# Kernel optimization log

Hardware: AMD Instinct MI355X
Metric: run time of the kernel (lower is better)

The kernel has to match this reference:

```python
import jax, jax.numpy as jnp
import numpy as np

HIDDEN = 1024
HEADS = 16
HEAD_DIM = HIDDEN // HEADS
EPS = 1e-6


def _layernorm(x, gamma, beta):
    mu = jnp.mean(x, axis=-1, keepdims=True)
    var = jnp.mean(jnp.square(x - mu), axis=-1, keepdims=True)
    return (x - mu) * jax.lax.rsqrt(var + EPS) * gamma + beta


def setup_inputs() -> dict:
    key = jax.random.key(0)
    ks = jax.random.split(key, 16)
    B, S, D = 2, 2048, HIDDEN
    s = 1.0 / np.sqrt(D)
    inp = {
        "x": jax.random.normal(ks[0], (B, S, D), dtype=jnp.float32),
        "Wq": jax.random.uniform(ks[1], (D, D), jnp.float32, -s, s),
        "bq": jnp.zeros((D,), jnp.float32),
        "Wk": jax.random.uniform(ks[2], (D, D), jnp.float32, -s, s),
        "bk": jnp.zeros((D,), jnp.float32),
        "Wv": jax.random.uniform(ks[3], (D, D), jnp.float32, -s, s),
        "bv": jnp.zeros((D,), jnp.float32),
        "Wo": jax.random.uniform(ks[4], (D, D), jnp.float32, -s, s),
        "bo": jnp.zeros((D,), jnp.float32),
        "g1": jnp.ones((D,), jnp.float32),
        "b1": jnp.zeros((D,), jnp.float32),
        "Wup": jax.random.uniform(ks[5], (D, 4 * D), jnp.float32, -s, s),
        "bup": jnp.zeros((4 * D,), jnp.float32),
        "Wdn": jax.random.uniform(ks[6], (4 * D, D), jnp.float32, -0.5 * s, 0.5 * s),
        "bdn": jnp.zeros((D,), jnp.float32),
        "g2": jnp.ones((D,), jnp.float32),
        "b2": jnp.zeros((D,), jnp.float32),
    }
    return inp


def _forward(x, Wq, bq, Wk, bk, Wv, bv, Wo, bo, g1, b1, Wup, bup, Wdn, bdn, g2, b2):
    B, S, D = x.shape
    H, Hd = HEADS, HEAD_DIM
    # projections -> (B, H, S, Hd)
    q = (x @ Wq + bq).reshape(B, S, H, Hd).transpose(0, 2, 1, 3)
    k = (x @ Wk + bk).reshape(B, S, H, Hd).transpose(0, 2, 1, 3)
    v = (x @ Wv + bv).reshape(B, S, H, Hd).transpose(0, 2, 1, 3)
    # full NxN scores (faithful to the source: explicit QK^T, mask, softmax, AV)
    scores = jnp.einsum("bhqd,bhkd->bhqk", q, k) / np.sqrt(Hd)
    causal = jnp.tril(jnp.ones((S, S), dtype=bool))  # (S, S)
    scores = jnp.where(causal, scores, jnp.float32(-1e20))
    attn = jax.nn.softmax(scores, axis=-1)
    # dropout is identity in eval mode
    mid = jnp.einsum("bhqk,bhkd->bqhd", attn, v).reshape(B, S, D)
    attn_out = mid @ Wo + bo
    x = _layernorm(x + attn_out, g1, b1)
    # FFN
    up = jax.nn.relu(x @ Wup + bup)
    down = up @ Wdn + bdn
    return _layernorm(x + down, g2, b2)


def reference(x, Wq, bq, Wk, bk, Wv, bv, Wo, bo, g1, b1, Wup, bup, Wdn, bdn, g2, b2):
    return _forward(x, Wq, bq, Wk, bk, Wv, bv, Wo, bo, g1, b1, Wup, bup, Wdn, bdn, g2, b2)
```

## Files before the change

kernel.cpp:

```cpp
#include <hip/hip_runtime.h>

#define D_MODEL 1024
#define D_FFN   4096
#define SEQ     2048
#define NROWS   4096
#define QKV_LD  3072

typedef __bf16 bf16x8 __attribute__((ext_vector_type(8)));
typedef float  floatx4 __attribute__((ext_vector_type(4)));

#define MFMA_BF16 __builtin_amdgcn_mfma_f32_16x16x32_bf16

__device__ __forceinline__ unsigned short f2bf(float f) {
  unsigned int u = __float_as_uint(f);
  u += 0x7FFFu + ((u >> 16) & 1u);
  return (unsigned short)(u >> 16);
}

template <int C>
__device__ __forceinline__ float ror16(float x) {
  return __int_as_float(
      __builtin_amdgcn_mov_dpp(__float_as_int(x), 0x120 | C, 0xf, 0xf, true));
}

__device__ __forceinline__ void async16(const unsigned short* g, unsigned short* l) {
  __builtin_amdgcn_global_load_lds(
      (const __attribute__((address_space(1))) unsigned int*)g,
      (__attribute__((address_space(3))) unsigned int*)l, 16, 0, 0);
}

__global__ __launch_bounds__(256) void k_f32_to_bf16(
    const float* __restrict__ in, unsigned short* __restrict__ outp, long n) {
  long i = ((long)blockIdx.x * 256 + threadIdx.x) * 4;
  if (i >= n) return;
  float4 v = *(const float4*)(in + i);
  ushort4 o;
  o.x = f2bf(v.x); o.y = f2bf(v.y); o.z = f2bf(v.z); o.w = f2bf(v.w);
  *(ushort4*)(outp + i) = o;
}

__global__ __launch_bounds__(256) void k_transpose_bf16(
    const float* __restrict__ W, unsigned short* __restrict__ WT, int R, int C) {
  __shared__ float tile[32][33];
  int tx = threadIdx.x & 31, ty = threadIdx.x >> 5;
  long bx = (long)blockIdx.x * 32;
  long by = (long)blockIdx.y * 32;
  #pragma unroll
  for (int j = 0; j < 4; j++)
    tile[ty + j * 8][tx] = W[(by + ty + j * 8) * C + bx + tx];
  __syncthreads();
  #pragma unroll
  for (int j = 0; j < 4; j++)
    WT[(bx + ty + j * 8) * R + by + tx] = f2bf(tile[tx][ty + j * 8]);
}

__global__ __launch_bounds__(256) void k_transpose_sq(
    const float* __restrict__ Wq, const float* __restrict__ Wk,
    const float* __restrict__ Wv, const float* __restrict__ Wo,
    unsigned short* __restrict__ WqkvT, unsigned short* __restrict__ WoT) {
  __shared__ float tile[32][33];
  int z = blockIdx.z;
  const float* W = (z == 0) ? Wq : (z == 1) ? Wk : (z == 2) ? Wv : Wo;
  unsigned short* dst = (z < 3) ? (WqkvT + (size_t)z * D_MODEL * D_MODEL) : WoT;
  int tx = threadIdx.x & 31, ty = threadIdx.x >> 5;
  long bx = (long)blockIdx.x * 32;
  long by = (long)blockIdx.y * 32;
  #pragma unroll
  for (int j = 0; j < 4; j++)
    tile[ty + j * 8][tx] = W[(by + ty + j * 8) * D_MODEL + bx + tx];
  __syncthreads();
  #pragma unroll
  for (int j = 0; j < 4; j++)
    dst[(bx + ty + j * 8) * D_MODEL + by + tx] = f2bf(tile[tx][ty + j * 8]);
}

__global__ __launch_bounds__(256) void k_pack_bias(
    const float* __restrict__ bq, const float* __restrict__ bk,
    const float* __restrict__ bv, float* __restrict__ dst) {
  int i = blockIdx.x * 256 + threadIdx.x;
  if (i >= 3072) return;
  float v = (i < 1024) ? bq[i] : (i < 2048) ? bk[i - 1024] : bv[i - 2048];
  dst[i] = v;
}

__global__ __launch_bounds__(256) void k_transpose_v(
    const unsigned short* __restrict__ QKV, unsigned short* __restrict__ Vt) {
  __shared__ unsigned short tile[64][72];
  int r0 = blockIdx.x * 64;
  int c0 = blockIdx.y * 64;
  int tx = threadIdx.x & 15, ty = threadIdx.x >> 4;
  #pragma unroll
  for (int j = 0; j < 4; j++) {
    int r = ty + j * 16;
    *(ushort4*)&tile[r][tx * 4] =
        *(const ushort4*)(QKV + (long)(r0 + r) * QKV_LD + 2048 + c0 + tx * 4);
  }
  __syncthreads();
  #pragma unroll
  for (int j = 0; j < 4; j++) {
    int d = ty + j * 16;
    ushort4 o;
    o.x = tile[tx * 4 + 0][d];
    o.y = tile[tx * 4 + 1][d];
    o.z = tile[tx * 4 + 2][d];
    o.w = tile[tx * 4 + 3][d];
    *(ushort4*)(Vt + (long)(c0 + d) * NROWS + r0 + tx * 4) = o;
  }
}

__global__ __launch_bounds__(512, 4) void k_gemm128(
    const unsigned short* __restrict__ A,
    const unsigned short* __restrict__ Bt,
    const float* __restrict__ bias,
    void* __restrict__ Cp, int M, int N, int K, int flags) {
  __shared__ unsigned short lds[2 * 16384];
  int tid = threadIdx.x, lane = tid & 63, wave = tid >> 6;
  int quad = lane >> 4, l16 = lane & 15;
  int wm = wave >> 2, wn = wave & 3;

  int gx = gridDim.x;
  int nwg = gx * gridDim.y;
  int orig = blockIdx.y * gx + blockIdx.x;
  int wg = (orig & 7) * (nwg >> 3) + (orig >> 3);
  long bm = (long)(wg % gx) * 128;
  long bn = (long)(wg / gx) * 128;

  int T = K / 64;

  const floatx4 fz = {0.f, 0.f, 0.f, 0.f};
  floatx4 acc[4][2];
  #pragma unroll
  for (int i = 0; i < 4; i++)
    #pragma unroll
    for (int j = 0; j < 2; j++) acc[i][j] = fz;

  int srow = tid >> 3;
  int sc = (tid & 7) ^ (srow & 7);
  const unsigned short* Ag = A + (bm + srow) * (long)K + sc * 8;
  const unsigned short* Bg = Bt + (bn + srow) * (long)K + sc * 8;

  auto stage = [&](int tt, int c) {
    unsigned short* An = lds + c * 16384;
    unsigned short* Bn = An + 8192;
    long ko = (long)tt * 64;
    async16(Ag + ko, An + wave * 512);
    async16(Ag + 64 * (long)K + ko, An + 4096 + wave * 512);
    async16(Bg + ko, Bn + wave * 512);
    async16(Bg + 64 * (long)K + ko, Bn + 4096 + wave * 512);
  };

  int aoff = (wm * 64 + l16) * 64;
  int boff = (wn * 32 + l16) * 64;
  int sw = l16 & 7;
  int ca0 = (quad ^ sw) * 8;
  int ca1 = ((4 + quad) ^ sw) * 8;

  stage(0, 0);
  for (int t = 0; t < T; t++) {
    int c = t & 1;
    const unsigned short* Ac = lds + c * 16384;
    const unsigned short* Bc = Ac + 8192;
    int tn = (t + 1 < T) ? t + 1 : T - 1;
    stage(tn, c ^ 1);
    __asm__ volatile("s_waitcnt vmcnt(4)" ::: "memory");
    __builtin_amdgcn_s_barrier();

    bf16x8 af[4][2], bfr[2][2];
    #pragma unroll
    for (int m = 0; m < 4; m++) {
      af[m][0] = *(const bf16x8*)(Ac + aoff + m * 1024 + ca0);
      af[m][1] = *(const bf16x8*)(Ac + aoff + m * 1024 + ca1);
    }
    #pragma unroll
    for (int n = 0; n < 2; n++) {
      bfr[n][0] = *(const bf16x8*)(Bc + boff + n * 1024 + ca0);
      bfr[n][1] = *(const bf16x8*)(Bc + boff + n * 1024 + ca1);
    }
    __asm__ volatile("s_waitcnt lgkmcnt(0)" ::: "memory");
    __builtin_amdgcn_s_setprio(1);
    #pragma unroll
    for (int h = 0; h < 2; h++)
      #pragma unroll
      for (int m = 0; m < 4; m++)
        #pragma unroll
        for (int n = 0; n < 2; n++)
          acc[m][n] = MFMA_BF16(af[m][h], bfr[n][h], acc[m][n], 0, 0, 0);
    __builtin_amdgcn_s_setprio(0);
    __builtin_amdgcn_s_barrier();
  }

  bool f32out = (flags & 1) != 0;
  bool relu   = (flags & 2) != 0;
  float* outf = (float*)Cp;
  unsigned short* outh = (unsigned short*)Cp;
  #pragma unroll
  for (int n = 0; n < 2; n++) {
    long col = bn + wn * 32 + n * 16 + l16;
    float bvv = bias[col];
    #pragma unroll
    for (int m = 0; m < 4; m++) {
      long row = bm + wm * 64 + m * 16 + quad * 4;
      #pragma unroll
      for (int r = 0; r < 4; r++) {
        float v = acc[m][n][r] + bvv;
        if (relu) v = fmaxf(v, 0.0f);
        if (f32out) outf[(row + r) * (long)N + col] = v;
        else        outh[(row + r) * (long)N + col] = f2bf(v);
      }
    }
  }
}

__global__ __launch_bounds__(512, 2) void k_gemm256(
    const unsigned short* __restrict__ A,
    const unsigned short* __restrict__ Bt,
    const float* __restrict__ bias,
    void* __restrict__ Cp, int M, int N, int K, int flags) {
  extern __shared__ unsigned short lds[];
  int tid = threadIdx.x, lane = tid & 63, wave = tid >> 6;
  int quad = lane >> 4, l16 = lane & 15;
  int wm = wave >> 2, wn = wave & 3;

  int nwg = gridDim.x * gridDim.y;
  int orig = blockIdx.y * gridDim.x + blockIdx.x;
  int wg = (orig & 7) * (nwg >> 3) + (orig >> 3);
  long bm = (long)(wg & 15) * 256;
  long bn = (long)(wg >> 4) * 256;

  int z = blockIdx.z;
  int Ks = K / gridDim.z;
  long zb = (long)z * Ks;
  int T = Ks / 64;

  const floatx4 fz = {0.f, 0.f, 0.f, 0.f};
  floatx4 acc[8][4];
  #pragma unroll
  for (int i = 0; i < 8; i++)
    #pragma unroll
    for (int j = 0; j < 4; j++) acc[i][j] = fz;

  int srow = tid >> 3;
  int sc = (tid & 7) ^ (srow & 7);
  const unsigned short* Ag = A + (bm + srow) * (long)K + zb + sc * 8;
  const unsigned short* Bg = Bt + (bn + srow) * (long)K + zb + sc * 8;

  auto stage = [&](int tt, int c) {
    unsigned short* An = lds + c * 32768;
    unsigned short* Bn = An + 16384;
    long ko = (long)tt * 64;
    #pragma unroll
    for (int i = 0; i < 4; i++) {
      async16(Ag + (long)i * 64 * K + ko, An + i * 4096 + wave * 512);
      async16(Bg + (long)i * 64 * K + ko, Bn + i * 4096 + wave * 512);
    }
  };

  int aoff = (wm * 128 + l16) * 64;
  int boff = (wn * 64 + l16) * 64;
  int sw = l16 & 7;
  int ca0 = (quad ^ sw) * 8;
  int ca1 = ((4 + quad) ^ sw) * 8;

  stage(0, 0);
  for (int t = 0; t < T; t++) {
    int c = t & 1;
    const unsigned short* Ac = lds + c * 32768;
    const unsigned short* Bc = Ac + 16384;
    int tn = (t + 1 < T) ? t + 1 : T - 1;
    stage(tn, c ^ 1);
    __asm__ volatile("s_waitcnt vmcnt(8)" ::: "memory");
    __builtin_amdgcn_s_barrier();

    bf16x8 af[8], b0, b1;
    #pragma unroll
    for (int m = 0; m < 8; m++) af[m] = *(const bf16x8*)(Ac + aoff + m * 1024 + ca0);
    b0 = *(const bf16x8*)(Bc + boff + 0 * 1024 + ca0);
    b1 = *(const bf16x8*)(Bc + boff + 1 * 1024 + ca0);
    __asm__ volatile("s_waitcnt lgkmcnt(0)" ::: "memory");
    __builtin_amdgcn_s_setprio(1);
    #pragma unroll
    for (int m = 0; m < 8; m++) acc[m][0] = MFMA_BF16(af[m], b0, acc[m][0], 0, 0, 0);
    #pragma unroll
    for (int m = 0; m < 8; m++) acc[m][1] = MFMA_BF16(af[m], b1, acc[m][1], 0, 0, 0);
    __builtin_amdgcn_s_setprio(0);
    __builtin_amdgcn_s_barrier();
    b0 = *(const bf16x8*)(Bc + boff + 2 * 1024 + ca0);
    b1 = *(const bf16x8*)(Bc + boff + 3 * 1024 + ca0);
    __asm__ volatile("s_waitcnt lgkmcnt(0)" ::: "memory");
    __builtin_amdgcn_s_setprio(1);
    #pragma unroll
    for (int m = 0; m < 8; m++) acc[m][2] = MFMA_BF16(af[m], b0, acc[m][2], 0, 0, 0);
    #pragma unroll
    for (int m = 0; m < 8; m++) acc[m][3] = MFMA_BF16(af[m], b1, acc[m][3], 0, 0, 0);
    __builtin_amdgcn_s_setprio(0);
    __builtin_amdgcn_s_barrier();
    #pragma unroll
    for (int m = 0; m < 8; m++) af[m] = *(const bf16x8*)(Ac + aoff + m * 1024 + ca1);
    b0 = *(const bf16x8*)(Bc + boff + 0 * 1024 + ca1);
    b1 = *(const bf16x8*)(Bc + boff + 1 * 1024 + ca1);
    __asm__ volatile("s_waitcnt lgkmcnt(0)" ::: "memory");
    __builtin_amdgcn_s_setprio(1);
    #pragma unroll
    for (int m = 0; m < 8; m++) acc[m][0] = MFMA_BF16(af[m], b0, acc[m][0], 0, 0, 0);
    #pragma unroll
    for (int m = 0; m < 8; m++) acc[m][1] = MFMA_BF16(af[m], b1, acc[m][1], 0, 0, 0);
    __builtin_amdgcn_s_setprio(0);
    __builtin_amdgcn_s_barrier();
    b0 = *(const bf16x8*)(Bc + boff + 2 * 1024 + ca1);
    b1 = *(const bf16x8*)(Bc + boff + 3 * 1024 + ca1);
    __asm__ volatile("s_waitcnt lgkmcnt(0)" ::: "memory");
    __builtin_amdgcn_s_setprio(1);
    #pragma unroll
    for (int m = 0; m < 8; m++) acc[m][2] = MFMA_BF16(af[m], b0, acc[m][2], 0, 0, 0);
    #pragma unroll
    for (int m = 0; m < 8; m++) acc[m][3] = MFMA_BF16(af[m], b1, acc[m][3], 0, 0, 0);
    __builtin_amdgcn_s_setprio(0);
    __builtin_amdgcn_s_barrier();
  }

  bool f32out = (flags & 1) != 0;
  bool relu   = (flags & 2) != 0;
  float* outf = (float*)Cp + (size_t)z * M * (size_t)N;
  unsigned short* outh = (unsigned short*)Cp;
  #pragma unroll
  for (int n = 0; n < 4; n++) {
    long col = bn + wn * 64 + n * 16 + l16;
    float bvv = (z == 0) ? bias[col] : 0.0f;
    #pragma unroll
    for (int m = 0; m < 8; m++) {
      long row = bm + wm * 128 + m * 16 + quad * 4;
      #pragma unroll
      for (int r = 0; r < 4; r++) {
        float v = acc[m][n][r] + bvv;
        if (relu) v = fmaxf(v, 0.0f);
        if (f32out) outf[(row + r) * (long)N + col] = v;
        else        outh[(row + r) * (long)N + col] = f2bf(v);
      }
    }
  }
}

#define PLD 72
__global__ __launch_bounds__(256) void k_attn(
    const unsigned short* __restrict__ QKV,
    const unsigned short* __restrict__ Vt,
    unsigned short* __restrict__ Omat) {
  __shared__ unsigned short Ks[64 * 64];
  __shared__ unsigned short Vs[64 * 64];
  __shared__ unsigned short Ps[4][16 * PLD];
  int tid = threadIdx.x;
  int lane = tid & 63, wave = tid >> 6;
  int quad = lane >> 4, l16 = lane & 15;
  int z = blockIdx.x;
  int bh = z & 31;
  int qp = z >> 5;
  int b = bh >> 4, h = bh & 15;
  long rowbase = (long)b * SEQ;
  int hd0 = h * 64;
  unsigned short* pw = &Ps[wave][0];
  const float SCL = 0.18033688f;
  const floatx4 fz = {0.f, 0.f, 0.f, 0.f};

  int r_in = lane >> 3;
  int cpos = lane & 7;

  bf16x8 ones;
  #pragma unroll
  for (int i = 0; i < 8; i++) ones[i] = (__bf16)1.0f;

  #pragma unroll
  for (int phase = 0; phase < 2; phase++) {
    int qt = phase ? qp : (31 - qp);
    int q0w = qt * 64 + wave * 16;
    int qrow = q0w + quad * 4;
    int ntiles = qt + 1;

    bf16x8 qf0, qf1;
    {
      const unsigned short* qp_ =
          QKV + (rowbase + q0w + l16) * (long)QKV_LD + hd0 + quad * 8;
      qf0 = *(const bf16x8*)(qp_);
      qf1 = *(const bf16x8*)(qp_ + 32);
    }

    floatx4 ao[4], aol;
    #pragma unroll
    for (int t = 0; t < 4; t++) ao[t] = fz;
    aol = fz;
    float m_i[4];
    #pragma unroll
    for (int r = 0; r < 4; r++) m_i[r] = -3.0e38f;

    for (int it = 0; it < ntiles; it++) {
      int kv0 = it << 6;
      #pragma unroll
      for (int jj = 0; jj < 2; jj++) {
        int j = wave * 2 + jj;
        int r = j * 8 + r_in;
        int c = cpos ^ (r & 7);
        const unsigned short* gk =
            QKV + (rowbase + kv0 + r) * (long)QKV_LD + 1024 + hd0 + c * 8;
        async16(gk, Ks + j * 512);
        const unsigned short* gv =
            Vt + (long)(hd0 + r) * NROWS + rowbase + kv0 + c * 8;
        async16(gv, Vs + j * 512);
      }
      __syncthreads();

      floatx4 sacc[4];
      #pragma unroll
      for (int t = 0; t < 4; t++) {
        int row = t * 16 + l16;
        int sw = row & 7;
        bf16x8 kf0 = *(const bf16x8*)(Ks + row * 64 + (quad ^ sw) * 8);
        bf16x8 kf1 = *(const bf16x8*)(Ks + row * 64 + ((quad + 4) ^ sw) * 8);
        sacc[t] = __builtin_amdgcn_mfma_f32_16x16x32_bf16(qf0, kf0, fz, 0, 0, 0);
        sacc[t] = __builtin_amdgcn_mfma_f32_16x16x32_bf16(qf1, kf1, sacc[t], 0, 0, 0);
      }

      bool maskt = (it == ntiles - 1);
      if (maskt) {
        #pragma unroll
        for (int t = 0; t < 4; t++) {
          int kvc = kv0 + t * 16 + l16;
          #pragma unroll
          for (int r = 0; r < 4; r++) {
            float s = sacc[t][r] * SCL;
            sacc[t][r] = (kvc > qrow + r) ? -1.0e30f : s;
          }
        }
      } else {
        #pragma unroll
        for (int t = 0; t < 4; t++)
          #pragma unroll
          for (int r = 0; r < 4; r++) sacc[t][r] *= SCL;
      }

      float Mg = sacc[0][0];
      #pragma unroll
      for (int t = 0; t < 4; t++)
        #pragma unroll
        for (int r = 0; r < 4; r++) Mg = fmaxf(Mg, sacc[t][r]);
      Mg = fmaxf(Mg, ror16<1>(Mg));
      Mg = fmaxf(Mg, ror16<2>(Mg));
      Mg = fmaxf(Mg, ror16<4>(Mg));
      Mg = fmaxf(Mg, ror16<8>(Mg));

      float alpha[4];
      #pragma unroll
      for (int r = 0; r < 4; r++) {
        float mn = fmaxf(m_i[r], Mg);
        alpha[r] = __builtin_amdgcn_exp2f(m_i[r] - mn);
        m_i[r] = mn;
      }

      #pragma unroll
      for (int t = 0; t < 4; t++)
        #pragma unroll
        for (int r = 0; r < 4; r++) {
          float p = __builtin_amdgcn_exp2f(sacc[t][r] - m_i[r]);
          pw[(quad * 4 + r) * PLD + t * 16 + l16] =
              (unsigned short)(__float_as_uint(p) >> 16);
        }

      #pragma unroll
      for (int t = 0; t < 4; t++)
        #pragma unroll
        for (int r = 0; r < 4; r++) ao[t][r] *= alpha[r];
      #pragma unroll
      for (int r = 0; r < 4; r++) aol[r] *= alpha[r];

      __asm__ volatile("s_waitcnt lgkmcnt(0)" ::: "memory");
      bf16x8 pf0 = *(const bf16x8*)(pw + l16 * PLD + quad * 8);
      bf16x8 pf1 = *(const bf16x8*)(pw + l16 * PLD + 32 + quad * 8);

      #pragma unroll
      for (int t = 0; t < 4; t++) {
        int row = t * 16 + l16;
        int sw = row & 7;
        bf16x8 vf0 = *(const bf16x8*)(Vs + row * 64 + (quad ^ sw) * 8);
        bf16x8 vf1 = *(const bf16x8*)(Vs + row * 64 + ((quad + 4) ^ sw) * 8);
        ao[t] = __builtin_amdgcn_mfma_f32_16x16x32_bf16(pf0, vf0, ao[t], 0, 0, 0);
        ao[t] = __builtin_amdgcn_mfma_f32_16x16x32_bf16(pf1, vf1, ao[t], 0, 0, 0);
      }
      aol = __builtin_amdgcn_mfma_f32_16x16x32_bf16(pf0, ones, aol, 0, 0, 0);
      aol = __builtin_amdgcn_mfma_f32_16x16x32_bf16(pf1, ones, aol, 0, 0, 0);

      __syncthreads();
    }

    float inv[4];
    #pragma unroll
    for (int r = 0; r < 4; r++) inv[r] = 1.0f / aol[r];
    #pragma unroll
    for (int t = 0; t < 4; t++)
      #pragma unroll
      for (int r = 0; r < 4; r++)
        Omat[(rowbase + qrow + r) * (long)D_MODEL + hd0 + t * 16 + l16] =
            f2bf(ao[t][r] * inv[r]);
  }
}

__global__ __launch_bounds__(256) void k_add_ln(
    const float* __restrict__ A, const float* __restrict__ P,
    const float* __restrict__ g, const float* __restrict__ be,
    float* __restrict__ Y, unsigned short* __restrict__ Ybf) {
  __shared__ float sb[4], ssb[4];
  int tid = threadIdx.x;
  long base = (long)blockIdx.x * D_MODEL + tid * 4;
  float4 a  = *(const float4*)(A + base);
  float4 p0 = *(const float4*)(P + base);
  float v0 = a.x + p0.x;
  float v1 = a.y + p0.y;
  float v2 = a.z + p0.z;
  float v3 = a.w + p0.w;
  float s  = v0 + v1 + v2 + v3;
  float ss = v0 * v0 + v1 * v1 + v2 * v2 + v3 * v3;
  #pragma unroll
  for (int o = 32; o >= 1; o >>= 1) {
    s  += __shfl_xor(s, o, 64);
    ss += __shfl_xor(ss, o, 64);
  }
  int wave = tid >> 6;
  if ((tid & 63) == 0) { sb[wave] = s; ssb[wave] = ss; }
  __syncthreads();
  s  = sb[0] + sb[1] + sb[2] + sb[3];
  ss = ssb[0] + ssb[1] + ssb[2] + ssb[3];
  float mu  = s * (1.0f / 1024.0f);
  float var = ss * (1.0f / 1024.0f) - mu * mu;
  float rstd = rsqrtf(var + 1e-6f);
  float4 gv  = *(const float4*)(g + tid * 4);
  float4 bev = *(const float4*)(be + tid * 4);
  float o0 = (v0 - mu) * rstd * gv.x + bev.x;
  float o1 = (v1 - mu) * rstd * gv.y + bev.y;
  float o2 = (v2 - mu) * rstd * gv.z + bev.z;
  float o3 = (v3 - mu) * rstd * gv.w + bev.w;
  if (Y) *(float4*)(Y + base) = make_float4(o0, o1, o2, o3);
  if (Ybf) {
    ushort4 u;
    u.x = f2bf(o0); u.y = f2bf(o1); u.z = f2bf(o2); u.w = f2bf(o3);
    *(ushort4*)(Ybf + base) = u;
  }
}

extern "C" void kernel_launch(void* const* d_in, const int* in_sizes, int n_in,
                              void* d_out, int out_size, void* d_ws, size_t ws_size,
                              hipStream_t stream) {
  (void)in_sizes; (void)n_in; (void)out_size; (void)ws_size;
  static bool s_attr = false;
  if (!s_attr) {
    hipFuncSetAttribute((const void*)k_gemm256,
                        hipFuncAttributeMaxDynamicSharedMemorySize, 131072);
    s_attr = true;
  }
  const float* x   = (const float*)d_in[0];
  const float* Wq  = (const float*)d_in[1];
  const float* bq  = (const float*)d_in[2];
  const float* Wk  = (const float*)d_in[3];
  const float* bk  = (const float*)d_in[4];
  const float* Wv  = (const float*)d_in[5];
  const float* bv  = (const float*)d_in[6];
  const float* Wo  = (const float*)d_in[7];
  const float* bo  = (const float*)d_in[8];
  const float* g1  = (const float*)d_in[9];
  const float* b1  = (const float*)d_in[10];
  const float* Wup = (const float*)d_in[11];
  const float* bup = (const float*)d_in[12];
  const float* Wdn = (const float*)d_in[13];
  const float* bdn = (const float*)d_in[14];
  const float* g2  = (const float*)d_in[15];
  const float* b2  = (const float*)d_in[16];
  float* out = (float*)d_out;

  char* ws = (char*)d_ws;
  size_t off = 0;
  auto alloc = [&](size_t bytes) {
    char* p = ws + off;
    off = (off + bytes + 255) & ~(size_t)255;
    return p;
  };
  unsigned short* x_bf   = (unsigned short*)alloc((size_t)NROWS * D_MODEL * 2);
  unsigned short* WqkvT  = (unsigned short*)alloc((size_t)QKV_LD * D_MODEL * 2);
  unsigned short* WoT    = (unsigned short*)alloc((size_t)D_MODEL * D_MODEL * 2);
  unsigned short* WupT   = (unsigned short*)alloc((size_t)D_FFN * D_MODEL * 2);
  unsigned short* WdnT   = (unsigned short*)alloc((size_t)D_MODEL * D_FFN * 2);
  float*          bqkv   = (float*)alloc((size_t)QKV_LD * 4);
  unsigned short* qkv_bf = (unsigned short*)alloc((size_t)NROWS * QKV_LD * 2);
  unsigned short* Vt     = (unsigned short*)alloc((size_t)D_MODEL * NROWS * 2);
  unsigned short* mid_bf = (unsigned short*)alloc((size_t)NROWS * D_MODEL * 2);
  float*          x1f    = (float*)alloc((size_t)NROWS * D_MODEL * 4);
  unsigned short* x1bf   = (unsigned short*)alloc((size_t)NROWS * D_MODEL * 2);
  float*          part   = (float*)alloc((size_t)NROWS * D_MODEL * 4);
  unsigned short* h_bf   = (unsigned short*)alloc((size_t)NROWS * D_FFN * 2);

  k_f32_to_bf16<<<4096, 256, 0, stream>>>(x, x_bf, (long)NROWS * D_MODEL);
  k_transpose_sq<<<dim3(32, 32, 4), 256, 0, stream>>>(Wq, Wk, Wv, Wo, WqkvT, WoT);
  k_transpose_bf16<<<dim3(128, 32), 256, 0, stream>>>(Wup, WupT, D_MODEL, D_FFN);
  k_transpose_bf16<<<dim3(32, 128), 256, 0, stream>>>(Wdn, WdnT, D_FFN, D_MODEL);
  k_pack_bias<<<12, 256, 0, stream>>>(bq, bk, bv, bqkv);

  k_gemm128<<<dim3(32, 24), 512, 0, stream>>>(x_bf, WqkvT, bqkv, qkv_bf,
                                              NROWS, QKV_LD, D_MODEL, 0);
  k_transpose_v<<<dim3(64, 16), 256, 0, stream>>>(qkv_bf, Vt);

  k_attn<<<512, 256, 0, stream>>>(qkv_bf, Vt, mid_bf);

  k_gemm128<<<dim3(32, 8), 512, 0, stream>>>(mid_bf, WoT, bo, part,
                                             NROWS, D_MODEL, D_MODEL, 1);
  k_add_ln<<<4096, 256, 0, stream>>>(x, part, g1, b1, x1f, x1bf);

  k_gemm256<<<dim3(16, 16, 1), 512, 131072, stream>>>(x1bf, WupT, bup, h_bf,
                                                      NROWS, D_FFN, D_MODEL, 2);
  k_gemm128<<<dim3(32, 8), 512, 0, stream>>>(h_bf, WdnT, bdn, part,
                                             NROWS, D_MODEL, D_FFN, 1);
  k_add_ln<<<4096, 256, 0, stream>>>(x1f, part, g2, b2, out, nullptr);
}
```

Baseline: 363.2 us.

## Split attention into one q-tile per block and add lazy softmax rescaling

Each attention block used to process a pair of q-tiles (long and short) in two phases. It now handles a single q-tile, with the grid doubled to 1024 blocks and the longest tiles scheduled first. This gives more parallelism at the cost of relying on the hardware scheduler for load balance. The softmax scale is folded into an FMA inside exp2, and the running max and accumulators are only rescaled when the new tile max exceeds the old max by more than a threshold. That skips most alpha multiplies but lets unnormalized values grow by up to 2^8 before rescaling.

```diff
diff --git a/kernel.cpp b/kernel.cpp
--- a/kernel.cpp
+++ b/kernel.cpp
@@ -353,7 +353,7 @@
   int quad = lane >> 4, l16 = lane & 15;
   int z = blockIdx.x;
   int bh = z & 31;
-  int qp = z >> 5;
+  int qt = 31 - (z >> 5);
   int b = bh >> 4, h = bh & 15;
   long rowbase = (long)b * SEQ;
   int hd0 = h * 64;
@@ -368,137 +368,124 @@
   #pragma unroll
   for (int i = 0; i < 8; i++) ones[i] = (__bf16)1.0f;
 
-  #pragma unroll
-  for (int phase = 0; phase < 2; phase++) {
-    int qt = phase ? qp : (31 - qp);
-    int q0w = qt * 64 + wave * 16;
-    int qrow = q0w + quad * 4;
-    int ntiles = qt + 1;
-
-    bf16x8 qf0, qf1;
-    {
-      const unsigned short* qp_ =
-          QKV + (rowbase + q0w + l16) * (long)QKV_LD + hd0 + quad * 8;
-      qf0 = *(const bf16x8*)(qp_);
-      qf1 = *(const bf16x8*)(qp_ + 32);
-    }
-
-    floatx4 ao[4], aol;
-    #pragma unroll
-    for (int t = 0; t < 4; t++) ao[t] = fz;
-    aol = fz;
-    float m_i[4];
-    #pragma unroll
-    for (int r = 0; r < 4; r++) m_i[r] = -3.0e38f;
-
-    for (int it = 0; it < ntiles; it++) {
-      int kv0 = it << 6;
-      #pragma unroll
-      for (int jj = 0; jj < 2; jj++) {
-        int j = wave * 2 + jj;
-        int r = j * 8 + r_in;
-        int c = cpos ^ (r & 7);
-        const unsigned short* gk =
-            QKV + (rowbase + kv0 + r) * (long)QKV_LD + 1024 + hd0 + c * 8;
-        async16(gk, Ks + j * 512);
-        const unsigned short* gv =
-            Vt + (long)(hd0 + r) * NROWS + rowbase + kv0 + c * 8;
-        async16(gv, Vs + j * 512);
-      }
-      __syncthreads();
-
-      floatx4 sacc[4];
+  int q0w = qt * 64 + wave * 16;
+  int qrow = q0w + quad * 4;
+  int ntiles = qt + 1;
+
+  bf16x8 qf0, qf1;
+  {
+    const unsigned short* qp_ =
+        QKV + (rowbase + q0w + l16) * (long)QKV_LD + hd0 + quad * 8;
+    qf0 = *(const bf16x8*)(qp_);
+    qf1 = *(const bf16x8*)(qp_ + 32);
+  }
+
+  floatx4 ao[4], aol;
+  #pragma unroll
+  for (int t = 0; t < 4; t++) ao[t] = fz;
+  aol = fz;
+  float m_i[4];
+  #pragma unroll
+  for (int r = 0; r < 4; r++) m_i[r] = -3.0e38f;
+
+  for (int it = 0; it < ntiles; it++) {
+    int kv0 = it << 6;
+    #pragma unroll
+    for (int jj = 0; jj < 2; jj++) {
+      int j = wave * 2 + jj;
+      int r = j * 8 + r_in;
+      int c = cpos ^ (r & 7);
+      const unsigned short* gk =
+          QKV + (rowbase + kv0 + r) * (long)QKV_LD + 1024 + hd0 + c * 8;
+      async16(gk, Ks + j * 512);
+      const unsigned short* gv =
+          Vt + (long)(hd0 + r) * NROWS + rowbase + kv0 + c * 8;
+      async16(gv, Vs + j * 512);
+    }
+    __syncthreads();
+
+    floatx4 sacc[4];
+    #pragma unroll
+    for (int t = 0; t < 4; t++) {
+      int row = t * 16 + l16;
+      int sw = row & 7;
+      bf16x8 kf0 = *(const bf16x8*)(Ks + row * 64 + (quad ^ sw) * 8);
+      bf16x8 kf1 = *(const bf16x8*)(Ks + row * 64 + ((quad + 4) ^ sw) * 8);
+      sacc[t] = __builtin_amdgcn_mfma_f32_16x16x32_bf16(qf0, kf0, fz, 0, 0, 0);
+      sacc[t] = __builtin_amdgcn_mfma_f32_16x16x32_bf16(qf1, kf1, sacc[t], 0, 0, 0);
+    }
+
+    if (it == ntiles - 1) {
       #pragma unroll
       for (int t = 0; t < 4; t++) {
-        int row = t * 16 + l16;
-        int sw = row & 7;
-        bf16x8 kf0 = *(const bf16x8*)(Ks + row * 64 + (quad ^ sw) * 8);
-        bf16x8 kf1 = *(const bf16x8*)(Ks + row * 64 + ((quad + 4) ^ sw) * 8);
-        sacc[t] = __builtin_amdgcn_mfma_f32_16x16x32_bf16(qf0, kf0, fz, 0, 0, 0);
-        sacc[t] = __builtin_amdgcn_mfma_f32_16x16x32_bf16(qf1, kf1, sacc[t], 0, 0, 0);
+        int kvc = kv0 + t * 16 + l16;
+        #pragma unroll
+        for (int r = 0; r < 4; r++)
+          sacc[t][r] = (kvc > qrow + r) ? -1.0e30f : sacc[t][r];
       }
-
-      bool maskt = (it == ntiles - 1);
-      if (maskt) {
-        #pragma unroll
-        for (int t = 0; t < 4; t++) {
-          int kvc = kv0 + t * 16 + l16;
-          #pragma unroll
-          for (int r = 0; r < 4; r++) {
-            float s = sacc[t][r] * SCL;
-            sacc[t][r] = (kvc > qrow + r) ? -1.0e30f : s;
-          }
-        }
-      } else {
-        #pragma unroll
-        for (int t = 0; t < 4; t++)
-          #pragma unroll
-          for (int r = 0; r < 4; r++) sacc[t][r] *= SCL;
-      }
-
-      float Mg = sacc[0][0];
+    }
+
+    float Mg = sacc[0][0];
+    #pragma unroll
+    for (int t = 0; t < 4; t++)
       #pragma unroll
-      for (int t = 0; t < 4; t++)
-        #pragma unroll
-        for (int r = 0; r < 4; r++) Mg = fmaxf(Mg, sacc[t][r]);
-      Mg = fmaxf(Mg, ror16<1>(Mg));
-      Mg = fmaxf(Mg, ror16<2>(Mg));
-      Mg = fmaxf(Mg, ror16<4>(Mg));
-      Mg = fmaxf(Mg, ror16<8>(Mg));
-
-      float alpha[4];
+      for (int r = 0; r < 4; r++) Mg = fmaxf(Mg, sacc[t][r]);
+    Mg = fmaxf(Mg, ror16<1>(Mg));
+    Mg = fmaxf(Mg, ror16<2>(Mg));
+    Mg = fmaxf(Mg, ror16<4>(Mg));
+    Mg = fmaxf(Mg, ror16<8>(Mg));
+    float Mg_s = Mg * SCL;
+
+    float m_min = fminf(fminf(m_i[0], m_i[1]), fminf(m_i[2], m_i[3]));
+    if (Mg_s > m_min + 8.0f) {
       #pragma unroll
       for (int r = 0; r < 4; r++) {
-        float mn = fmaxf(m_i[r], Mg);
-        alpha[r] = __builtin_amdgcn_exp2f(m_i[r] - mn);
+        float mn = fmaxf(m_i[r], Mg_s);
+        float alpha = __builtin_amdgcn_exp2f(m_i[r] - mn);
         m_i[r] = mn;
+        #pragma unroll
+        for (int t = 0; t < 4; t++) ao[t][r] *= alpha;
+        aol[r] *= alpha;
       }
-
-      #pragma unroll
-      for (int t = 0; t < 4; t++)
-        #pragma unroll
-        for (int r = 0; r < 4; r++) {
-          float p = __builtin_amdgcn_exp2f(sacc[t][r] - m_i[r]);
-          pw[(quad * 4 + r) * PLD + t * 16 + l16] =
-              (unsigned short)(__float_as_uint(p) >> 16);
-        }
-
-      #pragma unroll
-      for (int t = 0; t < 4; t++)
-        #pragma unroll
-        for (int r = 0; r < 4; r++) ao[t][r] *= alpha[r];
-      #pragma unroll
-      for (int r = 0; r < 4; r++) aol[r] *= alpha[r];
-
-      __asm__ volatile("s_waitcnt lgkmcnt(0)" ::: "memory");
-      bf16x8 pf0 = *(const bf16x8*)(pw + l16 * PLD + quad * 8);
-      bf16x8 pf1 = *(const bf16x8*)(pw + l16 * PLD + 32 + quad * 8);
-
-      #pragma unroll
-      for (int t = 0; t < 4; t++) {
-        int row = t * 16 + l16;
-        int sw = row & 7;
-        bf16x8 vf0 = *(const bf16x8*)(Vs + row * 64 + (quad ^ sw) * 8);
-        bf16x8 vf1 = *(const bf16x8*)(Vs + row * 64 + ((quad + 4) ^ sw) * 8);
-        ao[t] = __builtin_amdgcn_mfma_f32_16x16x32_bf16(pf0, vf0, ao[t], 0, 0, 0);
-        ao[t] = __builtin_amdgcn_mfma_f32_16x16x32_bf16(pf1, vf1, ao[t], 0, 0, 0);
-      }
-      aol = __builtin_amdgcn_mfma_f32_16x16x32_bf16(pf0, ones, aol, 0, 0, 0);
-      aol = __builtin_amdgcn_mfma_f32_16x16x32_bf16(pf1, ones, aol, 0, 0, 0);
-
-      __syncthreads();
-    }
-
-    float inv[4];
-    #pragma unroll
-    for (int r = 0; r < 4; r++) inv[r] = 1.0f / aol[r];
+    }
+
     #pragma unroll
     for (int t = 0; t < 4; t++)
       #pragma unroll
-      for (int r = 0; r < 4; r++)
-        Omat[(rowbase + qrow + r) * (long)D_MODEL + hd0 + t * 16 + l16] =
-            f2bf(ao[t][r] * inv[r]);
-  }
+      for (int r = 0; r < 4; r++) {
+        float p = __builtin_amdgcn_exp2f(fmaf(sacc[t][r], SCL, -m_i[r]));
+        pw[(quad * 4 + r) * PLD + t * 16 + l16] =
+            (unsigned short)(__float_as_uint(p) >> 16);
+      }
+
+    __asm__ volatile("s_waitcnt lgkmcnt(0)" ::: "memory");
+    bf16x8 pf0 = *(const bf16x8*)(pw + l16 * PLD + quad * 8);
+    bf16x8 pf1 = *(const bf16x8*)(pw + l16 * PLD + 32 + quad * 8);
+
+    #pragma unroll
+    for (int t = 0; t < 4; t++) {
+      int row = t * 16 + l16;
+      int sw = row & 7;
+      bf16x8 vf0 = *(const bf16x8*)(Vs + row * 64 + (quad ^ sw) * 8);
+      bf16x8 vf1 = *(const bf16x8*)(Vs + row * 64 + ((quad + 4) ^ sw) * 8);
+      ao[t] = __builtin_amdgcn_mfma_f32_16x16x32_bf16(pf0, vf0, ao[t], 0, 0, 0);
+      ao[t] = __builtin_amdgcn_mfma_f32_16x16x32_bf16(pf1, vf1, ao[t], 0, 0, 0);
+    }
+    aol = __builtin_amdgcn_mfma_f32_16x16x32_bf16(pf0, ones, aol, 0, 0, 0);
+    aol = __builtin_amdgcn_mfma_f32_16x16x32_bf16(pf1, ones, aol, 0, 0, 0);
+
+    __syncthreads();
+  }
+
+  float inv[4];
+  #pragma unroll
+  for (int r = 0; r < 4; r++) inv[r] = 1.0f / aol[r];
+  #pragma unroll
+  for (int t = 0; t < 4; t++)
+    #pragma unroll
+    for (int r = 0; r < 4; r++)
+      Omat[(rowbase + qrow + r) * (long)D_MODEL + hd0 + t * 16 + l16] =
+          f2bf(ao[t][r] * inv[r]);
 }
 
 __global__ __launch_bounds__(256) void k_add_ln(
@@ -603,7 +590,7 @@
                                               NROWS, QKV_LD, D_MODEL, 0);
   k_transpose_v<<<dim3(64, 16), 256, 0, stream>>>(qkv_bf, Vt);
 
-  k_attn<<<512, 256, 0, stream>>>(qkv_bf, Vt, mid_bf);
+  k_attn<<<1024, 256, 0, stream>>>(qkv_bf, Vt, mid_bf);
 
   k_gemm128<<<dim3(32, 8), 512, 0, stream>>>(mid_bf, WoT, bo, part,
                                              NROWS, D_MODEL, D_MODEL, 1);
```

Measured after the change: 372.0 us. 2.4% more time.
